# Kernel tuning notes

Measured on AMD Instinct MI355X. Metric: run time of the kernel, lower is better.

## Reference

```python
import jax, jax.numpy as jnp
import numpy as np


def _filters():
    ident = jnp.array([[0., 0., 0.], [0., 1., 0.], [0., 0., 0.]], jnp.float32)
    sobel_x = jnp.array([[-1., 0., 1.], [-2., 0., 2.], [-1., 0., 1.]], jnp.float32)
    lap = jnp.array([[1., 2., 1.], [2., -12., 2.], [1., 2., 1.]], jnp.float32)
    return jnp.stack([ident, sobel_x, sobel_x.T, lap])  # [4,3,3]


def _perception(x):
    # depthwise conv with 4 fixed filters, circular padding; matches torch
    # reshape(b*ch,1,h,w) -> conv -> reshape(b, ch*4, h, w) channel ordering
    b, c, h, w = x.shape
    xp = jnp.pad(x, ((0, 0), (0, 0), (1, 1), (1, 1)), mode='wrap')
    y = xp.reshape(b * c, 1, h + 2, w + 2)
    k = _filters()[:, None]  # [4,1,3,3]
    y = jax.lax.conv_general_dilated(
        y, k, window_strides=(1, 1), padding='VALID',
        dimension_numbers=('NCHW', 'OIHW', 'NCHW'))  # [b*c,4,h,w]
    return y.reshape(b, c * 4, h, w)


def setup_inputs() -> dict:
    key = jax.random.key(0)
    k1, k2, k3, k4, k5 = jax.random.split(key, 5)
    B, C, H, W = 32, 12, 256, 256
    FC = 96
    xavier_std = 0.2 * np.sqrt(2.0 / (4 * C + FC))  # xavier_normal gain=0.2
    return {
        'x': jax.random.normal(k1, (B, C, H, W), jnp.float32),
        'w1': jax.random.normal(k2, (FC, 4 * C), jnp.float32) * xavier_std,
        'b1': jax.random.normal(k3, (FC,), jnp.float32) * 0.01,
        'w2': jax.random.normal(k4, (C, FC), jnp.float32) * 0.02,
        'rand_mask': jax.random.uniform(k5, (B, 1, H, W), jnp.float32),
    }


def reference(x, w1, b1, w2, rand_mask):
    update_rate = 0.5
    y = _perception(x)  # [B, 4C, H, W]
    hidden = jax.nn.relu(jnp.einsum('oc,bchw->bohw', w1, y) + b1[None, :, None, None])
    y = jnp.einsum('oc,bchw->bohw', w2, hidden)  # [B, C, H, W]
    update_mask = jnp.floor(rand_mask + update_rate)  # bernoulli(update_rate)
    return x + y * update_mask
```

## Files before the change

kernel.cpp:

```cpp
#include <hip/hip_runtime.h>
#include <stdint.h>

#define NC 12
#define NHW (256*256)
#define RSTR 136
#define CSTR 840

typedef __attribute__((ext_vector_type(8))) short bf16x8;
typedef __attribute__((ext_vector_type(4))) float f32x4;
typedef __attribute__((ext_vector_type(4))) uint32_t u32x4;
typedef __attribute__((ext_vector_type(2))) __bf16 bf16x2v;

__device__ __forceinline__ uint32_t pkbf(float lo, float hi) {
    bf16x2v v = { (__bf16)lo, (__bf16)hi };
    return __builtin_bit_cast(uint32_t, v);
}
#define PIN(v) asm volatile("" : "+v"(v))

__global__ __launch_bounds__(256, 3) void nca_fused8(
    const float* __restrict__ x, const float* __restrict__ w1,
    const float* __restrict__ b1, const float* __restrict__ w2,
    const float* __restrict__ rmask, float* __restrict__ out)
{
    __shared__ float smem[12 * CSTR];

    const int tid  = threadIdx.x;
    const int lane = tid & 63;
    const int wv   = tid >> 6;
    const int g    = lane >> 4;
    const int p    = lane & 15;
    const int c0   = 3 * g;

    u32x4 a1u[6][2];
    f32x4 biasv[6];
    #pragma unroll
    for (int t = 0; t < 6; ++t) {
        const int row = 16*t + p;
        const float4 fa = *reinterpret_cast<const float4*>(w1 + row*48 + 12*g + 0);
        const float4 fb = *reinterpret_cast<const float4*>(w1 + row*48 + 12*g + 4);
        const float4 fc = *reinterpret_cast<const float4*>(w1 + row*48 + 12*g + 8);
        a1u[t][0] = (u32x4){ pkbf(fa.x, fa.y), pkbf(fa.z, fa.w), pkbf(fb.x, fb.y), pkbf(fb.z, fb.w) };
        a1u[t][1] = (u32x4){ pkbf(fc.x, fc.y), pkbf(fc.z, fc.w), 0u, 0u };
        biasv[t] = *reinterpret_cast<const f32x4*>(b1 + 16*t + 4*g);
        PIN(a1u[t][0]); PIN(a1u[t][1]); PIN(biasv[t]);
    }
    u32x4 a2u[3];
    #pragma unroll
    for (int s = 0; s < 3; ++s) {
        u32x4 u = {0u, 0u, 0u, 0u};
        if (p < NC) {
            const float4 wa = *reinterpret_cast<const float4*>(w2 + p*96 + 32*s + 4*g);
            const float4 wb = *reinterpret_cast<const float4*>(w2 + p*96 + 32*s + 16 + 4*g);
            u = (u32x4){ pkbf(wa.x, wa.y), pkbf(wa.z, wa.w), pkbf(wb.x, wb.y), pkbf(wb.z, wb.w) };
        }
        a2u[s] = u;
        PIN(a2u[s]);
    }

    const int b     = blockIdx.x >> 7;
    const int strip = (blockIdx.x >> 1) & 63;
    const int half  = blockIdx.x & 1;
    const int ra    = strip << 2;
    const int c0g   = half << 7;
    const float* __restrict__ xb = x + (size_t)b * NC * NHW;
    const float* __restrict__ mb = rmask + (size_t)b * NHW;
    float* __restrict__ ob = out + (size_t)b * NC * NHW;

    {
        const int q = tid >> 5;
        const int l = tid & 31;
        #pragma unroll
        for (int j = 0; j < 9; ++j) {
            const int hr  = 8*j + q;
            const int c   = hr / 6;
            const int r   = hr - 6*c;
            const int row = (ra + 255 + r) & 255;
            const f32x4 v = *reinterpret_cast<const f32x4*>(xb + c*NHW + (row << 8) + c0g + (l << 2));
            *reinterpret_cast<f32x4*>(&smem[c*CSTR + r*RSTR + 4 + (l << 2)]) = v;
        }
        if (tid < 144) {
            const int hr  = tid >> 1;
            const int side= tid & 1;
            const int c   = hr / 6;
            const int r   = hr - 6*c;
            const int row = (ra + 255 + r) & 255;
            const int col = side ? ((c0g + 128) & 255) : ((c0g + 255) & 255);
            smem[c*CSTR + r*RSTR + (side ? 132 : 3)] = xb[c*NHW + (row << 8) + col];
        }
    }
    __syncthreads();

    const int h    = ra + wv;
    const int hrow = h << 8;

    #pragma unroll 2
    for (int grp = 0; grp < 8; ++grp) {
        const int wcl = (grp << 4) + p;
        const int wcg = c0g + wcl;

        uint32_t yw[6];
        #pragma unroll
        for (int ci = 0; ci < 3; ++ci) {
            const float* t0 = &smem[(c0 + ci)*CSTR + (wv + 0)*RSTR + 3 + wcl];
            const float* t1 = &smem[(c0 + ci)*CSTR + (wv + 1)*RSTR + 3 + wcl];
            const float* t2 = &smem[(c0 + ci)*CSTR + (wv + 2)*RSTR + 3 + wcl];
            const float v0 = t0[0], v1 = t0[1], v2 = t0[2];
            const float v3 = t1[0], v4 = t1[1], v5 = t1[2];
            const float v6 = t2[0], v7 = t2[1], v8 = t2[2];
            const float fsx = (v2 - v0) + 2.f*(v5 - v3) + (v8 - v6);
            const float fsy = (v6 - v0) + 2.f*(v7 - v1) + (v8 - v2);
            const float flp = ((v0 + v2) + (v6 + v8)) + 2.f*((v1 + v3) + (v5 + v7)) - 12.f*v4;
            yw[2*ci]   = pkbf(v4, fsx);
            yw[2*ci+1] = pkbf(fsy, flp);
        }
        const bf16x8 yf0 = __builtin_bit_cast(bf16x8, (u32x4){yw[0], yw[1], yw[2], yw[3]});
        const bf16x8 yf1 = __builtin_bit_cast(bf16x8, (u32x4){yw[4], yw[5], 0u, 0u});

        __builtin_amdgcn_s_setprio(1);
        uint32_t pu[6][2];
        #pragma unroll
        for (int t = 0; t < 6; ++t) {
            f32x4 acc = biasv[t];
            acc = __builtin_amdgcn_mfma_f32_16x16x32_bf16(__builtin_bit_cast(bf16x8, a1u[t][0]), yf0, acc, 0, 0, 0);
            acc = __builtin_amdgcn_mfma_f32_16x16x32_bf16(__builtin_bit_cast(bf16x8, a1u[t][1]), yf1, acc, 0, 0, 0);
            pu[t][0] = pkbf(fmaxf(acc[0], 0.f), fmaxf(acc[1], 0.f));
            pu[t][1] = pkbf(fmaxf(acc[2], 0.f), fmaxf(acc[3], 0.f));
        }
        f32x4 acc2 = {0.f, 0.f, 0.f, 0.f};
        #pragma unroll
        for (int s2 = 0; s2 < 3; ++s2) {
            const u32x4 fb2 = { pu[2*s2][0], pu[2*s2][1], pu[2*s2+1][0], pu[2*s2+1][1] };
            acc2 = __builtin_amdgcn_mfma_f32_16x16x32_bf16(__builtin_bit_cast(bf16x8, a2u[s2]), __builtin_bit_cast(bf16x8, fb2), acc2, 0, 0, 0);
        }
        __builtin_amdgcn_s_setprio(0);

        const float um = floorf(mb[hrow + wcg] + 0.5f);
        if (g < 3) {
            #pragma unroll
            for (int r = 0; r < 4; ++r) {
                const float xv = smem[(4*g + r)*CSTR + (wv + 1)*RSTR + 4 + wcl];
                ob[(4*g + r)*NHW + hrow + wcg] = xv + acc2[r] * um;
            }
        }
    }
}

extern "C" void kernel_launch(void* const* d_in, const int* in_sizes, int n_in,
                              void* d_out, int out_size, void* d_ws, size_t ws_size,
                              hipStream_t stream) {
    const float* x  = (const float*)d_in[0];
    const float* w1 = (const float*)d_in[1];
    const float* b1 = (const float*)d_in[2];
    const float* w2 = (const float*)d_in[3];
    const float* rm = (const float*)d_in[4];
    float* out = (float*)d_out;
    nca_fused8<<<dim3(32 * 64 * 2), dim3(256), 0, stream>>>(x, w1, b1, w2, rm, out);
}
```

Baseline: 86.90 us.

## Spread epilogue across all lane groups via permuted w2 rows, raise occupancy

```diff
diff --git a/kernel.cpp b/kernel.cpp
--- a/kernel.cpp
+++ b/kernel.cpp
@@ -17,7 +17,7 @@
 }
 #define PIN(v) asm volatile("" : "+v"(v))
 
-__global__ __launch_bounds__(256, 3) void nca_fused8(
+__global__ __launch_bounds__(256, 4) void nca_fused9(
     const float* __restrict__ x, const float* __restrict__ w1,
     const float* __restrict__ b1, const float* __restrict__ w2,
     const float* __restrict__ rmask, float* __restrict__ out)
@@ -45,16 +45,20 @@
         PIN(a1u[t][0]); PIN(a1u[t][1]); PIN(biasv[t]);
     }
     u32x4 a2u[3];
-    #pragma unroll
-    for (int s = 0; s < 3; ++s) {
-        u32x4 u = {0u, 0u, 0u, 0u};
-        if (p < NC) {
-            const float4 wa = *reinterpret_cast<const float4*>(w2 + p*96 + 32*s + 4*g);
-            const float4 wb = *reinterpret_cast<const float4*>(w2 + p*96 + 32*s + 16 + 4*g);
-            u = (u32x4){ pkbf(wa.x, wa.y), pkbf(wa.z, wa.w), pkbf(wb.x, wb.y), pkbf(wb.z, wb.w) };
+    {
+        const int rp = p & 3, gp = p >> 2;
+        const int chA = 4*rp + ((gp + rp) & 3);
+        #pragma unroll
+        for (int s = 0; s < 3; ++s) {
+            u32x4 u = {0u, 0u, 0u, 0u};
+            if (rp < 3) {
+                const float4 wa = *reinterpret_cast<const float4*>(w2 + chA*96 + 32*s + 4*g);
+                const float4 wb = *reinterpret_cast<const float4*>(w2 + chA*96 + 32*s + 16 + 4*g);
+                u = (u32x4){ pkbf(wa.x, wa.y), pkbf(wa.z, wa.w), pkbf(wb.x, wb.y), pkbf(wb.z, wb.w) };
+            }
+            a2u[s] = u;
+            PIN(a2u[s]);
         }
-        a2u[s] = u;
-        PIN(a2u[s]);
     }
 
     const int b     = blockIdx.x >> 7;
@@ -93,20 +97,32 @@
     const int h    = ra + wv;
     const int hrow = h << 8;
 
-    #pragma unroll 2
+    const float* tp[3][3];
+    #pragma unroll
+    for (int ci = 0; ci < 3; ++ci)
+        #pragma unroll
+        for (int q = 0; q < 3; ++q)
+            tp[ci][q] = &smem[(c0 + ci)*CSTR + (wv + q)*RSTR + 3 + p];
+    const float* xepi[3];
+    float*       obp[3];
+    #pragma unroll
+    for (int r = 0; r < 3; ++r) {
+        const int ch = 4*r + ((g + r) & 3);
+        xepi[r] = &smem[ch*CSTR + (wv + 1)*RSTR + 4 + p];
+        obp[r]  = ob + ch*NHW + hrow + c0g + p;
+    }
+    const float* mbp = mb + hrow + c0g + p;
+
+    #pragma unroll
     for (int grp = 0; grp < 8; ++grp) {
-        const int wcl = (grp << 4) + p;
-        const int wcg = c0g + wcl;
+        const int o = grp << 4;
 
         uint32_t yw[6];
         #pragma unroll
         for (int ci = 0; ci < 3; ++ci) {
-            const float* t0 = &smem[(c0 + ci)*CSTR + (wv + 0)*RSTR + 3 + wcl];
-            const float* t1 = &smem[(c0 + ci)*CSTR + (wv + 1)*RSTR + 3 + wcl];
-            const float* t2 = &smem[(c0 + ci)*CSTR + (wv + 2)*RSTR + 3 + wcl];
-            const float v0 = t0[0], v1 = t0[1], v2 = t0[2];
-            const float v3 = t1[0], v4 = t1[1], v5 = t1[2];
-            const float v6 = t2[0], v7 = t2[1], v8 = t2[2];
+            const float v0 = tp[ci][0][o+0], v1 = tp[ci][0][o+1], v2 = tp[ci][0][o+2];
+            const float v3 = tp[ci][1][o+0], v4 = tp[ci][1][o+1], v5 = tp[ci][1][o+2];
+            const float v6 = tp[ci][2][o+0], v7 = tp[ci][2][o+1], v8 = tp[ci][2][o+2];
             const float fsx = (v2 - v0) + 2.f*(v5 - v3) + (v8 - v6);
             const float fsy = (v6 - v0) + 2.f*(v7 - v1) + (v8 - v2);
             const float flp = ((v0 + v2) + (v6 + v8)) + 2.f*((v1 + v3) + (v5 + v7)) - 12.f*v4;
@@ -134,14 +150,10 @@
         }
         __builtin_amdgcn_s_setprio(0);
 
-        const float um = floorf(mb[hrow + wcg] + 0.5f);
-        if (g < 3) {
-            #pragma unroll
-            for (int r = 0; r < 4; ++r) {
-                const float xv = smem[(4*g + r)*CSTR + (wv + 1)*RSTR + 4 + wcl];
-                ob[(4*g + r)*NHW + hrow + wcg] = xv + acc2[r] * um;
-            }
-        }
+        const float um = floorf(mbp[o] + 0.5f);
+        #pragma unroll
+        for (int r = 0; r < 3; ++r)
+            obp[r][o] = xepi[r][o] + acc2[r] * um;
     }
 }
 
@@ -154,5 +166,5 @@
     const float* w2 = (const float*)d_in[3];
     const float* rm = (const float*)d_in[4];
     float* out = (float*)d_out;
-    nca_fused8<<<dim3(32 * 64 * 2), dim3(256), 0, stream>>>(x, w1, b1, w2, rm, out);
+    nca_fused9<<<dim3(32 * 64 * 2), dim3(256), 0, stream>>>(x, w1, b1, w2, rm, out);
 }
```

Result: no change. 86.29 us (-0.7%).
